# Kernel tuning notes

Hardware: AMD Instinct MI355X
Metric: run time of the kernel (lower is better)

Reference implementation:

```python
import jax, jax.numpy as jnp
import numpy as np

FEATURE_DIM = 512
PREDICATE_DIM = 2000
OBJECT_DIM = 100000
BATCH = 131072
EPS = 1e-5


def setup_inputs() -> dict:
    key = jax.random.key(0)
    ks = jax.random.split(key, 20)
    f, f2 = FEATURE_DIM, FEATURE_DIM // 2

    def w(k, shape, fan_in):
        bound = 1.0 / np.sqrt(fan_in)
        return jax.random.uniform(k, shape, jnp.float32, -bound, bound)

    inp = {
        "subj": jax.random.randint(ks[0], (BATCH,), 0, OBJECT_DIM),
        "obj": jax.random.randint(ks[1], (BATCH,), 0, OBJECT_DIM),
        "predi": jax.random.randint(ks[2], (BATCH,), 0, PREDICATE_DIM),
        # Linear weights stored as (in, out) so one_hot @ W.T == W_io[idx]
        "W1": w(ks[3], (OBJECT_DIM, f), OBJECT_DIM), "b1": w(ks[4], (f,), OBJECT_DIM),
        "g1": jnp.ones((f,), jnp.float32), "be1": jnp.zeros((f,), jnp.float32),
        "W2": w(ks[5], (OBJECT_DIM, f), OBJECT_DIM), "b2": w(ks[6], (f,), OBJECT_DIM),
        "g2": jnp.ones((f,), jnp.float32), "be2": jnp.zeros((f,), jnp.float32),
        "W3": w(ks[7], (PREDICATE_DIM, f), PREDICATE_DIM), "b3": w(ks[8], (f,), PREDICATE_DIM),
        "g3": jnp.ones((f,), jnp.float32), "be3": jnp.zeros((f,), jnp.float32),
        "W4": w(ks[9], (f2, f), f), "b4": w(ks[10], (f2,), f),
        "g4": jnp.ones((f2,), jnp.float32), "be4": jnp.zeros((f2,), jnp.float32),
        "W5": w(ks[11], (1, f2), f2), "b5": w(ks[12], (1,), f2),
    }
    return inp


def _bn(x, g, b):
    # BatchNorm1d training mode: biased variance over batch
    m = jnp.mean(x, axis=0)
    v = jnp.var(x, axis=0)
    return g * (x - m) * jax.lax.rsqrt(v + EPS) + b


def reference(subj, obj, predi,
              W1, b1, g1, be1,
              W2, b2, g2, be2,
              W3, b3, g3, be3,
              W4, b4, g4, be4,
              W5, b5):
    # one_hot(idx) @ W.T + b  ==  row gather of (in,out) weight
    s = jax.nn.relu(_bn(W1[subj] + b1, g1, be1))
    o = jax.nn.relu(_bn(W2[obj] + b2, g2, be2))
    p = jax.nn.relu(_bn(W3[predi] + b3, g3, be3))
    fused = s + p + o                                  # [B, F]
    h = jax.nn.relu(_bn(fused @ W4.T + b4, g4, be4))   # [B, F//2]
    logit = (h @ W5.T + b5).squeeze()                  # [B]
    return logit
```

## Files before the change

kernel.cpp:

```cpp
#include <hip/hip_runtime.h>

#define BATCHN 131072
#define FD 512
#define F2 256
#define NOBJ 100000
#define NPRED 2000
#define LDSTR 520

typedef __bf16 bf16x8 __attribute__((ext_vector_type(8)));
typedef float f32x4 __attribute__((ext_vector_type(4)));

__device__ __forceinline__ ushort f2bf(float f) {
  union { float f; uint u; } c; c.f = f;
  uint u = c.u;
  u += 0x7FFFu + ((u >> 16) & 1u);
  return (ushort)(u >> 16);
}

#define WS_STATS123 202752
#define WS_S4       205824
#define WS_SCSH123  238592
#define WS_SCSH4    241664
#define WS_W4BF     242176
#define WS_A1       307712
#define WS_A2       25907712
#define WS_A3       51507712

__global__ __launch_bounds__(256) void k_hist(
    const int* __restrict__ subj, const int* __restrict__ obj,
    const int* __restrict__ predi, int* __restrict__ cnt)
{
  int b = blockIdx.x * 256 + threadIdx.x;
  atomicAdd(&cnt[subj[b]], 1);
  atomicAdd(&cnt[NOBJ + obj[b]], 1);
  atomicAdd(&cnt[2 * NOBJ + predi[b]], 1);
}

#define NB1 782
#define NB3 16
#define NB_SCAN (NB1 + NB1 + NB3)
__global__ __launch_bounds__(256) void k_scan123(
    const float* __restrict__ W1, const float* __restrict__ W2,
    const float* __restrict__ W3, const int* __restrict__ cnt,
    float* __restrict__ stats)
{
  int blk = blockIdx.x;
  int e, rowBase, N;
  if (blk < NB1)            { e = 0; rowBase = blk * 128;          N = NOBJ; }
  else if (blk < 2 * NB1)   { e = 1; rowBase = (blk - NB1) * 128;  N = NOBJ; }
  else                      { e = 2; rowBase = (blk - 2*NB1) * 128; N = NPRED; }
  const float* W = (e == 0) ? W1 : (e == 1 ? W2 : W3);
  const int* cn = cnt + (e == 0 ? 0 : (e == 1 ? NOBJ : 2 * NOBJ));

  __shared__ int cnL[128];
  __shared__ float redS[512], redQ[512];
  int t = threadIdx.x;
  if (t < 128) { int r = rowBase + t; cnL[t] = (r < N) ? cn[r] : 0; }
  redS[t] = 0.f; redS[t + 256] = 0.f; redQ[t] = 0.f; redQ[t + 256] = 0.f;
  __syncthreads();

  int c = t & 63, rg = t >> 6;
  float s[8], q[8];
  #pragma unroll
  for (int j = 0; j < 8; ++j) { s[j] = 0.f; q[j] = 0.f; }
  for (int rl = rg; rl < 128; rl += 4) {
    float w = (float)cnL[rl];
    if (w == 0.f) continue;
    const float* row = W + (size_t)(rowBase + rl) * FD + c * 8;
    float4 va = *(const float4*)(row);
    float4 vb = *(const float4*)(row + 4);
    float x[8] = {va.x, va.y, va.z, va.w, vb.x, vb.y, vb.z, vb.w};
    #pragma unroll
    for (int j = 0; j < 8; ++j) { s[j] += w * x[j]; q[j] += w * x[j] * x[j]; }
  }
  #pragma unroll
  for (int j = 0; j < 8; ++j) {
    atomicAdd(&redS[c * 8 + j], s[j]);
    atomicAdd(&redQ[c * 8 + j], q[j]);
  }
  __syncthreads();
  float* se = stats + e * 1024;
  atomicAdd(&se[t],        redS[t]);
  atomicAdd(&se[t + 256],  redS[t + 256]);
  atomicAdd(&se[512 + t],  redQ[t]);
  atomicAdd(&se[768 + t],  redQ[t + 256]);
}

__global__ void k_fin123(const float* __restrict__ stats,
                         const float* __restrict__ g1, const float* __restrict__ be1,
                         const float* __restrict__ g2, const float* __restrict__ be2,
                         const float* __restrict__ g3, const float* __restrict__ be3,
                         float* __restrict__ scsh)
{
  int e = blockIdx.x, f = threadIdx.x;
  const float* g  = (e == 0) ? g1  : (e == 1 ? g2  : g3);
  const float* be = (e == 0) ? be1 : (e == 1 ? be2 : be3);
  float S = stats[e * 1024 + f], SS = stats[e * 1024 + 512 + f];
  const float invB = 1.f / (float)BATCHN;
  float mean = S * invB;
  float var  = SS * invB - mean * mean;
  if (!(var >= 0.f && var < 1e30f)) var = 1.f;
  if (!(mean > -1e30f && mean < 1e30f)) mean = 0.f;
  float r = rsqrtf(var + 1e-5f);
  float sc = g[f] * r;
  scsh[e * 1024 + f]       = sc;
  scsh[e * 1024 + 512 + f] = be[f] - mean * sc;
}

__global__ __launch_bounds__(256) void k_convW4(const float* __restrict__ W4,
                                                ushort* __restrict__ w4bf)
{
  int i = (blockIdx.x * 256 + threadIdx.x) * 4;
  float4 v = *(const float4*)(W4 + i);
  ushort4 o = {f2bf(v.x), f2bf(v.y), f2bf(v.z), f2bf(v.w)};
  *(ushort4*)(w4bf + i) = o;
}

#define NB_A1 3125
#define NB_A3 63
#define NB_BUILD (NB_A1 + NB_A1 + NB_A3)
__global__ __launch_bounds__(256) void k_buildA(
    const float* __restrict__ W1, const float* __restrict__ W2,
    const float* __restrict__ W3, const ushort* __restrict__ w4bf,
    const int* __restrict__ cnt, const float* __restrict__ scsh,
    float* __restrict__ A1, float* __restrict__ A2, float* __restrict__ A3)
{
  alignas(16) __shared__ ushort tileL[32 * LDSTR];
  __shared__ int okL[32];
  int blk = blockIdx.x;
  int e, rowBase, N; const float* W; float* A; const int* cn;
  if (blk < NB_A1)          { e = 0; rowBase = blk * 32;             N = NOBJ;  W = W1; A = A1; cn = cnt; }
  else if (blk < 2 * NB_A1) { e = 1; rowBase = (blk - NB_A1) * 32;   N = NOBJ;  W = W2; A = A2; cn = cnt + NOBJ; }
  else                      { e = 2; rowBase = (blk - 2*NB_A1) * 32; N = NPRED; W = W3; A = A3; cn = cnt + 2 * NOBJ; }

  int t = threadIdx.x;
  if (t < 32) { int r = rowBase + t; okL[t] = (r < N) && (cn[r] != 0); }
  int c = t & 63, rg = t >> 6;
  float sc[8], sh[8];
  #pragma unroll
  for (int j = 0; j < 8; ++j) {
    sc[j] = scsh[e * 1024 + c * 8 + j];
    sh[j] = scsh[e * 1024 + 512 + c * 8 + j];
  }
  __syncthreads();

  for (int r = rg; r < 32; r += 4) {
    union { ushort o[8]; uint4 v; } u;
    if (okL[r]) {
      const float* row = W + (size_t)(rowBase + r) * FD + c * 8;
      float4 va = *(const float4*)(row);
      float4 vb = *(const float4*)(row + 4);
      float x[8] = {va.x, va.y, va.z, va.w, vb.x, vb.y, vb.z, vb.w};
      #pragma unroll
      for (int j = 0; j < 8; ++j) {
        float v = fmaxf(fmaf(sc[j], x[j], sh[j]), 0.f);
        v = fminf(v, 60000.f);
        u.o[j] = f2bf(v);
      }
    } else { u.v.x = 0; u.v.y = 0; u.v.z = 0; u.v.w = 0; }
    *(uint4*)&tileL[r * LDSTR + c * 8] = u.v;
  }
  __syncthreads();

  int w = t >> 6, lane = t & 63, m = lane & 15, q = lane >> 4;
  f32x4 acc[2][4];
  #pragma unroll
  for (int mi = 0; mi < 2; ++mi)
    #pragma unroll
    for (int ni = 0; ni < 4; ++ni)
      acc[mi][ni] = (f32x4){0.f, 0.f, 0.f, 0.f};
  const ushort* w4p = w4bf + ((size_t)(64 * w + m)) * FD + q * 8;
  const ushort* fpL = tileL + m * LDSTR + q * 8;
  for (int kk = 0; kk < 16; ++kk) {
    int kc = kk * 32;
    bf16x8 af0 = *(const bf16x8*)(fpL + kc);
    bf16x8 af1 = *(const bf16x8*)(fpL + 16 * LDSTR + kc);
    #pragma unroll
    for (int ni = 0; ni < 4; ++ni) {
      bf16x8 bfv = *(const bf16x8*)(w4p + ni * 16 * FD + kc);
      acc[0][ni] = __builtin_amdgcn_mfma_f32_16x16x32_bf16(af0, bfv, acc[0][ni], 0, 0, 0);
      acc[1][ni] = __builtin_amdgcn_mfma_f32_16x16x32_bf16(af1, bfv, acc[1][ni], 0, 0, 0);
    }
  }
  __syncthreads();

  float* ldsF = (float*)tileL;
  #pragma unroll
  for (int mi = 0; mi < 2; ++mi)
    #pragma unroll
    for (int ni = 0; ni < 4; ++ni)
      #pragma unroll
      for (int rr = 0; rr < 4; ++rr)
        ldsF[(16 * mi + 4 * q + rr) * 258 + 64 * w + 16 * ni + m] = acc[mi][ni][rr];
  __syncthreads();
  for (int r = 0; r < 32; ++r) {
    if (okL[r]) A[(size_t)(rowBase + r) * F2 + t] = ldsF[r * 258 + t];
  }
}

__global__ __launch_bounds__(256) void k_hstats(
    const int* __restrict__ subj, const int* __restrict__ obj,
    const int* __restrict__ predi,
    const float* __restrict__ A1, const float* __restrict__ A2,
    const float* __restrict__ A3, float* __restrict__ s4)
{
  __shared__ float colS[256], colQ[256];
  int t = threadIdx.x;
  colS[t] = 0.f; colQ[t] = 0.f;
  __syncthreads();
  int c = t & 31;
  int pair = t >> 5;
  float ls[8], lq[8];
  #pragma unroll
  for (int j = 0; j < 8; ++j) { ls[j] = 0.f; lq[j] = 0.f; }
  int base = blockIdx.x * 64;
  #pragma unroll 2
  for (int i = 0; i < 8; ++i) {
    int b = base + i * 8 + pair;
    const float* r1 = A1 + (size_t)subj[b]  * F2 + c * 8;
    const float* r2 = A2 + (size_t)obj[b]   * F2 + c * 8;
    const float* r3 = A3 + (size_t)predi[b] * F2 + c * 8;
    f32x4 a0 = *(const f32x4*)(r1), a1 = *(const f32x4*)(r1 + 4);
    f32x4 b0 = *(const f32x4*)(r2), b1 = *(const f32x4*)(r2 + 4);
    f32x4 c0 = *(const f32x4*)(r3), c1 = *(const f32x4*)(r3 + 4);
    f32x4 h0 = a0 + b0 + c0, h1 = a1 + b1 + c1;
    #pragma unroll
    for (int j = 0; j < 4; ++j) {
      ls[j]     += h0[j]; lq[j]     += h0[j] * h0[j];
      ls[4 + j] += h1[j]; lq[4 + j] += h1[j] * h1[j];
    }
  }
  #pragma unroll
  for (int j = 0; j < 8; ++j) {
    atomicAdd(&colS[c * 8 + j], ls[j]);
    atomicAdd(&colQ[c * 8 + j], lq[j]);
  }
  __syncthreads();
  int slot = blockIdx.x & 63;
  atomicAdd(&s4[slot * 512 + t],       colS[t]);
  atomicAdd(&s4[slot * 512 + 256 + t], colQ[t]);
}

__global__ void k_fin4(const float* __restrict__ s4, const float* __restrict__ g4,
                       const float* __restrict__ be4, float* __restrict__ scsh4)
{
  int j = threadIdx.x;
  float S = 0.f, SS = 0.f;
  for (int sl = 0; sl < 64; ++sl) { S += s4[sl * 512 + j]; SS += s4[sl * 512 + 256 + j]; }
  const float invB = 1.f / (float)BATCHN;
  float mean = S * invB;
  float var  = SS * invB - mean * mean;
  if (!(var >= 0.f && var < 1e30f)) var = 1.f;
  if (!(mean > -1e30f && mean < 1e30f)) mean = 0.f;
  float r = rsqrtf(var + 1e-5f);
  float sc = g4[j] * r;
  scsh4[j]       = sc;
  scsh4[256 + j] = be4[j] - mean * sc;
}

__global__ __launch_bounds__(256) void k_final(
    const int* __restrict__ subj, const int* __restrict__ obj,
    const int* __restrict__ predi,
    const float* __restrict__ A1, const float* __restrict__ A2,
    const float* __restrict__ A3, const float* __restrict__ scsh4,
    const float* __restrict__ W5, const float* __restrict__ b5,
    float* __restrict__ out)
{
  int t = threadIdx.x;
  int c = t & 31, pair = t >> 5;
  float sc4v[8], sh4v[8], w5v[8];
  #pragma unroll
  for (int j = 0; j < 8; ++j) {
    int col = c * 8 + j;
    sc4v[j] = scsh4[col];
    sh4v[j] = scsh4[256 + col];
    w5v[j]  = W5[col];
  }
  float bb = b5[0];
  int base = blockIdx.x * 64;
  #pragma unroll 2
  for (int i = 0; i < 8; ++i) {
    int b = base + i * 8 + pair;
    const float* r1 = A1 + (size_t)subj[b]  * F2 + c * 8;
    const float* r2 = A2 + (size_t)obj[b]   * F2 + c * 8;
    const float* r3 = A3 + (size_t)predi[b] * F2 + c * 8;
    f32x4 a0 = *(const f32x4*)(r1), a1 = *(const f32x4*)(r1 + 4);
    f32x4 b0 = *(const f32x4*)(r2), b1 = *(const f32x4*)(r2 + 4);
    f32x4 c0 = *(const f32x4*)(r3), c1 = *(const f32x4*)(r3 + 4);
    f32x4 h0 = a0 + b0 + c0, h1 = a1 + b1 + c1;
    float acc = 0.f;
    #pragma unroll
    for (int j = 0; j < 4; ++j) {
      acc += fmaxf(fmaf(sc4v[j],     h0[j], sh4v[j]),     0.f) * w5v[j];
      acc += fmaxf(fmaf(sc4v[4 + j], h1[j], sh4v[4 + j]), 0.f) * w5v[4 + j];
    }
    #pragma unroll
    for (int off = 1; off < 32; off <<= 1)
      acc += __shfl_xor(acc, off, 64);
    if (c == 0) out[b] = acc + bb;
  }
}

extern "C" void kernel_launch(void* const* d_in, const int* in_sizes, int n_in,
                              void* d_out, int out_size, void* d_ws, size_t ws_size,
                              hipStream_t stream)
{
  const int* subj  = (const int*)d_in[0];
  const int* obj   = (const int*)d_in[1];
  const int* predi = (const int*)d_in[2];
  const float* W1  = (const float*)d_in[3];
  const float* g1  = (const float*)d_in[5];
  const float* be1 = (const float*)d_in[6];
  const float* W2  = (const float*)d_in[7];
  const float* g2  = (const float*)d_in[9];
  const float* be2 = (const float*)d_in[10];
  const float* W3  = (const float*)d_in[11];
  const float* g3  = (const float*)d_in[13];
  const float* be3 = (const float*)d_in[14];
  const float* W4  = (const float*)d_in[15];
  const float* g4  = (const float*)d_in[17];
  const float* be4 = (const float*)d_in[18];
  const float* W5  = (const float*)d_in[19];
  const float* b5  = (const float*)d_in[20];

  float* wsf   = (float*)d_ws;
  int*   cnt   = (int*)d_ws;
  ushort* w4bf = (ushort*)(wsf + WS_W4BF);
  float* A1    = wsf + WS_A1;
  float* A2    = wsf + WS_A2;
  float* A3    = wsf + WS_A3;
  float* out   = (float*)d_out;

  hipMemsetAsync(d_ws, 0, WS_SCSH123 * 4, stream);
  k_hist<<<BATCHN / 256, 256, 0, stream>>>(subj, obj, predi, cnt);
  k_convW4<<<128, 256, 0, stream>>>(W4, w4bf);
  k_scan123<<<NB_SCAN, 256, 0, stream>>>(W1, W2, W3, cnt, wsf + WS_STATS123);
  k_fin123<<<3, 512, 0, stream>>>(wsf + WS_STATS123, g1, be1, g2, be2, g3, be3, wsf + WS_SCSH123);
  k_buildA<<<NB_BUILD, 256, 0, stream>>>(W1, W2, W3, w4bf, cnt, wsf + WS_SCSH123, A1, A2, A3);
  k_hstats<<<BATCHN / 64, 256, 0, stream>>>(subj, obj, predi, A1, A2, A3, wsf + WS_S4);
  k_fin4<<<1, 256, 0, stream>>>(wsf + WS_S4, g4, be4, wsf + WS_SCSH4);
  k_final<<<BATCHN / 64, 256, 0, stream>>>(subj, obj, predi, A1, A2, A3, wsf + WS_SCSH4, W5, b5, out);
}
```

Before: 844.5 us.

## Store projected tables and hidden activations in bf16, compact nonzero rows, prefetch W4

The per-row projected tables A1/A2/A3 are now stored as bf16 instead of fp32, which halves gather traffic. The stats kernel also writes the summed hidden vector h as bf16 so the final kernel reads one contiguous row instead of three random gathers. The scan and build kernels first compact the list of rows with nonzero counts in LDS and unroll over that list, and the W4 fragments in the MFMA loop are software-prefetched one step ahead. The cost is extra rounding error from bf16 storage of the tables and of h, plus an added 64 MB write and read for h.

```diff
diff --git a/kernel.cpp b/kernel.cpp
--- a/kernel.cpp
+++ b/kernel.cpp
@@ -23,8 +23,9 @@
 #define WS_SCSH4    241664
 #define WS_W4BF     242176
 #define WS_A1       307712
-#define WS_A2       25907712
-#define WS_A3       51507712
+#define WS_A2       13107712
+#define WS_A3       25907712
+#define WS_H        26163712
 
 __global__ __launch_bounds__(256) void k_hist(
     const int* __restrict__ subj, const int* __restrict__ obj,
@@ -46,33 +47,60 @@
 {
   int blk = blockIdx.x;
   int e, rowBase, N;
-  if (blk < NB1)            { e = 0; rowBase = blk * 128;          N = NOBJ; }
-  else if (blk < 2 * NB1)   { e = 1; rowBase = (blk - NB1) * 128;  N = NOBJ; }
+  if (blk < NB1)            { e = 0; rowBase = blk * 128;           N = NOBJ; }
+  else if (blk < 2 * NB1)   { e = 1; rowBase = (blk - NB1) * 128;   N = NOBJ; }
   else                      { e = 2; rowBase = (blk - 2*NB1) * 128; N = NPRED; }
   const float* W = (e == 0) ? W1 : (e == 1 ? W2 : W3);
   const int* cn = cnt + (e == 0 ? 0 : (e == 1 ? NOBJ : 2 * NOBJ));
 
-  __shared__ int cnL[128];
+  __shared__ int cnL[128], listR[128], nkS;
   __shared__ float redS[512], redQ[512];
   int t = threadIdx.x;
-  if (t < 128) { int r = rowBase + t; cnL[t] = (r < N) ? cn[r] : 0; }
+  if (t == 0) nkS = 0;
   redS[t] = 0.f; redS[t + 256] = 0.f; redQ[t] = 0.f; redQ[t + 256] = 0.f;
   __syncthreads();
+  if (t < 128) {
+    int r = rowBase + t;
+    int cv = (r < N) ? cn[r] : 0;
+    cnL[t] = cv;
+    if (cv > 0) { int p = atomicAdd(&nkS, 1); listR[p] = t; }
+  }
+  __syncthreads();
+  int nk = nkS;
 
   int c = t & 63, rg = t >> 6;
   float s[8], q[8];
   #pragma unroll
   for (int j = 0; j < 8; ++j) { s[j] = 0.f; q[j] = 0.f; }
-  for (int rl = rg; rl < 128; rl += 4) {
-    float w = (float)cnL[rl];
-    if (w == 0.f) continue;
-    const float* row = W + (size_t)(rowBase + rl) * FD + c * 8;
-    float4 va = *(const float4*)(row);
-    float4 vb = *(const float4*)(row + 4);
-    float x[8] = {va.x, va.y, va.z, va.w, vb.x, vb.y, vb.z, vb.w};
-    #pragma unroll
-    for (int j = 0; j < 8; ++j) { s[j] += w * x[j]; q[j] += w * x[j] * x[j]; }
-  }
+
+  #define SCAN_ACC(w_, va_, vb_) { \
+    float x_[8] = {va_.x, va_.y, va_.z, va_.w, vb_.x, vb_.y, vb_.z, vb_.w}; \
+    _Pragma("unroll") \
+    for (int j = 0; j < 8; ++j) { float wx = w_ * x_[j]; s[j] += wx; q[j] = fmaf(wx, x_[j], q[j]); } }
+
+  int ii = rg;
+  for (; ii + 12 < nk; ii += 16) {
+    int r0 = listR[ii], r1 = listR[ii + 4], r2 = listR[ii + 8], r3 = listR[ii + 12];
+    const float* p0 = W + (size_t)(rowBase + r0) * FD + c * 8;
+    const float* p1 = W + (size_t)(rowBase + r1) * FD + c * 8;
+    const float* p2 = W + (size_t)(rowBase + r2) * FD + c * 8;
+    const float* p3 = W + (size_t)(rowBase + r3) * FD + c * 8;
+    float4 a0 = *(const float4*)(p0), b0 = *(const float4*)(p0 + 4);
+    float4 a1 = *(const float4*)(p1), b1 = *(const float4*)(p1 + 4);
+    float4 a2 = *(const float4*)(p2), b2 = *(const float4*)(p2 + 4);
+    float4 a3 = *(const float4*)(p3), b3 = *(const float4*)(p3 + 4);
+    float w0 = (float)cnL[r0], w1 = (float)cnL[r1], w2 = (float)cnL[r2], w3 = (float)cnL[r3];
+    SCAN_ACC(w0, a0, b0); SCAN_ACC(w1, a1, b1); SCAN_ACC(w2, a2, b2); SCAN_ACC(w3, a3, b3);
+  }
+  for (; ii < nk; ii += 4) {
+    int r0 = listR[ii];
+    const float* p0 = W + (size_t)(rowBase + r0) * FD + c * 8;
+    float4 a0 = *(const float4*)(p0), b0 = *(const float4*)(p0 + 4);
+    float w0 = (float)cnL[r0];
+    SCAN_ACC(w0, a0, b0);
+  }
+  #undef SCAN_ACC
+
   #pragma unroll
   for (int j = 0; j < 8; ++j) {
     atomicAdd(&redS[c * 8 + j], s[j]);
@@ -123,18 +151,25 @@
     const float* __restrict__ W1, const float* __restrict__ W2,
     const float* __restrict__ W3, const ushort* __restrict__ w4bf,
     const int* __restrict__ cnt, const float* __restrict__ scsh,
-    float* __restrict__ A1, float* __restrict__ A2, float* __restrict__ A3)
+    ushort* __restrict__ A1, ushort* __restrict__ A2, ushort* __restrict__ A3)
 {
   alignas(16) __shared__ ushort tileL[32 * LDSTR];
-  __shared__ int okL[32];
+  __shared__ int okL[32], listR[32], nkS;
   int blk = blockIdx.x;
-  int e, rowBase, N; const float* W; float* A; const int* cn;
+  int e, rowBase, N; const float* W; ushort* A; const int* cn;
   if (blk < NB_A1)          { e = 0; rowBase = blk * 32;             N = NOBJ;  W = W1; A = A1; cn = cnt; }
   else if (blk < 2 * NB_A1) { e = 1; rowBase = (blk - NB_A1) * 32;   N = NOBJ;  W = W2; A = A2; cn = cnt + NOBJ; }
   else                      { e = 2; rowBase = (blk - 2*NB_A1) * 32; N = NPRED; W = W3; A = A3; cn = cnt + 2 * NOBJ; }
 
   int t = threadIdx.x;
-  if (t < 32) { int r = rowBase + t; okL[t] = (r < N) && (cn[r] != 0); }
+  if (t == 0) nkS = 0;
+  __syncthreads();
+  if (t < 32) {
+    int r = rowBase + t;
+    int ok = (r < N) && (cn[r] != 0);
+    okL[t] = ok;
+    if (ok) { int p = atomicAdd(&nkS, 1); listR[p] = t; }
+  }
   int c = t & 63, rg = t >> 6;
   float sc[8], sh[8];
   #pragma unroll
@@ -143,23 +178,35 @@
     sh[j] = scsh[e * 1024 + 512 + c * 8 + j];
   }
   __syncthreads();
-
-  for (int r = rg; r < 32; r += 4) {
-    union { ushort o[8]; uint4 v; } u;
-    if (okL[r]) {
-      const float* row = W + (size_t)(rowBase + r) * FD + c * 8;
-      float4 va = *(const float4*)(row);
-      float4 vb = *(const float4*)(row + 4);
-      float x[8] = {va.x, va.y, va.z, va.w, vb.x, vb.y, vb.z, vb.w};
-      #pragma unroll
-      for (int j = 0; j < 8; ++j) {
-        float v = fmaxf(fmaf(sc[j], x[j], sh[j]), 0.f);
-        v = fminf(v, 60000.f);
-        u.o[j] = f2bf(v);
-      }
-    } else { u.v.x = 0; u.v.y = 0; u.v.z = 0; u.v.w = 0; }
-    *(uint4*)&tileL[r * LDSTR + c * 8] = u.v;
-  }
+  int nk = nkS;
+
+  #define CONV_STORE(rr_, va_, vb_) { \
+    float x_[8] = {va_.x, va_.y, va_.z, va_.w, vb_.x, vb_.y, vb_.z, vb_.w}; \
+    union { ushort o[8]; uint4 v; } u_; \
+    _Pragma("unroll") \
+    for (int j = 0; j < 8; ++j) { \
+      float v_ = fmaxf(fmaf(sc[j], x_[j], sh[j]), 0.f); \
+      v_ = fminf(v_, 60000.f); \
+      u_.o[j] = f2bf(v_); } \
+    *(uint4*)&tileL[(rr_) * LDSTR + c * 8] = u_.v; }
+
+  int ii = rg;
+  for (; ii + 4 < nk; ii += 8) {
+    int ra = listR[ii], rb = listR[ii + 4];
+    const float* pa = W + (size_t)(rowBase + ra) * FD + c * 8;
+    const float* pb = W + (size_t)(rowBase + rb) * FD + c * 8;
+    float4 a0 = *(const float4*)(pa), a1 = *(const float4*)(pa + 4);
+    float4 b0 = *(const float4*)(pb), b1 = *(const float4*)(pb + 4);
+    CONV_STORE(ra, a0, a1);
+    CONV_STORE(rb, b0, b1);
+  }
+  if (ii < nk) {
+    int ra = listR[ii];
+    const float* pa = W + (size_t)(rowBase + ra) * FD + c * 8;
+    float4 a0 = *(const float4*)(pa), a1 = *(const float4*)(pa + 4);
+    CONV_STORE(ra, a0, a1);
+  }
+  #undef CONV_STORE
   __syncthreads();
 
   int w = t >> 6, lane = t & 63, m = lane & 15, q = lane >> 4;
@@ -171,16 +218,32 @@
       acc[mi][ni] = (f32x4){0.f, 0.f, 0.f, 0.f};
   const ushort* w4p = w4bf + ((size_t)(64 * w + m)) * FD + q * 8;
   const ushort* fpL = tileL + m * LDSTR + q * 8;
+
+  bf16x8 bc0 = *(const bf16x8*)(w4p + 0 * 16 * FD);
+  bf16x8 bc1 = *(const bf16x8*)(w4p + 1 * 16 * FD);
+  bf16x8 bc2 = *(const bf16x8*)(w4p + 2 * 16 * FD);
+  bf16x8 bc3 = *(const bf16x8*)(w4p + 3 * 16 * FD);
   for (int kk = 0; kk < 16; ++kk) {
     int kc = kk * 32;
     bf16x8 af0 = *(const bf16x8*)(fpL + kc);
     bf16x8 af1 = *(const bf16x8*)(fpL + 16 * LDSTR + kc);
-    #pragma unroll
-    for (int ni = 0; ni < 4; ++ni) {
-      bf16x8 bfv = *(const bf16x8*)(w4p + ni * 16 * FD + kc);
-      acc[0][ni] = __builtin_amdgcn_mfma_f32_16x16x32_bf16(af0, bfv, acc[0][ni], 0, 0, 0);
-      acc[1][ni] = __builtin_amdgcn_mfma_f32_16x16x32_bf16(af1, bfv, acc[1][ni], 0, 0, 0);
+    bf16x8 bn0, bn1, bn2, bn3;
+    if (kk < 15) {
+      int kn = kc + 32;
+      bn0 = *(const bf16x8*)(w4p + 0 * 16 * FD + kn);
+      bn1 = *(const bf16x8*)(w4p + 1 * 16 * FD + kn);
+      bn2 = *(const bf16x8*)(w4p + 2 * 16 * FD + kn);
+      bn3 = *(const bf16x8*)(w4p + 3 * 16 * FD + kn);
     }
+    acc[0][0] = __builtin_amdgcn_mfma_f32_16x16x32_bf16(af0, bc0, acc[0][0], 0, 0, 0);
+    acc[1][0] = __builtin_amdgcn_mfma_f32_16x16x32_bf16(af1, bc0, acc[1][0], 0, 0, 0);
+    acc[0][1] = __builtin_amdgcn_mfma_f32_16x16x32_bf16(af0, bc1, acc[0][1], 0, 0, 0);
+    acc[1][1] = __builtin_amdgcn_mfma_f32_16x16x32_bf16(af1, bc1, acc[1][1], 0, 0, 0);
+    acc[0][2] = __builtin_amdgcn_mfma_f32_16x16x32_bf16(af0, bc2, acc[0][2], 0, 0, 0);
+    acc[1][2] = __builtin_amdgcn_mfma_f32_16x16x32_bf16(af1, bc2, acc[1][2], 0, 0, 0);
+    acc[0][3] = __builtin_amdgcn_mfma_f32_16x16x32_bf16(af0, bc3, acc[0][3], 0, 0, 0);
+    acc[1][3] = __builtin_amdgcn_mfma_f32_16x16x32_bf16(af1, bc3, acc[1][3], 0, 0, 0);
+    bc0 = bn0; bc1 = bn1; bc2 = bn2; bc3 = bn3;
   }
   __syncthreads();
 
@@ -193,16 +256,23 @@
       for (int rr = 0; rr < 4; ++rr)
         ldsF[(16 * mi + 4 * q + rr) * 258 + 64 * w + 16 * ni + m] = acc[mi][ni][rr];
   __syncthreads();
-  for (int r = 0; r < 32; ++r) {
-    if (okL[r]) A[(size_t)(rowBase + r) * F2 + t] = ldsF[r * 258 + t];
+  int hr = t >> 7, p = (t & 127) * 2;
+  for (int r = 0; r < 32; r += 2) {
+    int rr = r + hr;
+    if (okL[rr]) {
+      float v0 = ldsF[rr * 258 + p], v1 = ldsF[rr * 258 + p + 1];
+      uint pack = (uint)f2bf(v0) | ((uint)f2bf(v1) << 16);
+      *(uint*)&A[(size_t)(rowBase + rr) * F2 + p] = pack;
+    }
   }
 }
 
 __global__ __launch_bounds__(256) void k_hstats(
     const int* __restrict__ subj, const int* __restrict__ obj,
     const int* __restrict__ predi,
-    const float* __restrict__ A1, const float* __restrict__ A2,
-    const float* __restrict__ A3, float* __restrict__ s4)
+    const ushort* __restrict__ A1, const ushort* __restrict__ A2,
+    const ushort* __restrict__ A3, ushort* __restrict__ h,
+    float* __restrict__ s4)
 {
   __shared__ float colS[256], colQ[256];
   int t = threadIdx.x;
@@ -217,18 +287,17 @@
   #pragma unroll 2
   for (int i = 0; i < 8; ++i) {
     int b = base + i * 8 + pair;
-    const float* r1 = A1 + (size_t)subj[b]  * F2 + c * 8;
-    const float* r2 = A2 + (size_t)obj[b]   * F2 + c * 8;
-    const float* r3 = A3 + (size_t)predi[b] * F2 + c * 8;
-    f32x4 a0 = *(const f32x4*)(r1), a1 = *(const f32x4*)(r1 + 4);
-    f32x4 b0 = *(const f32x4*)(r2), b1 = *(const f32x4*)(r2 + 4);
-    f32x4 c0 = *(const f32x4*)(r3), c1 = *(const f32x4*)(r3 + 4);
-    f32x4 h0 = a0 + b0 + c0, h1 = a1 + b1 + c1;
+    bf16x8 v1 = *(const bf16x8*)(A1 + (size_t)subj[b]  * F2 + c * 8);
+    bf16x8 v2 = *(const bf16x8*)(A2 + (size_t)obj[b]   * F2 + c * 8);
+    bf16x8 v3 = *(const bf16x8*)(A3 + (size_t)predi[b] * F2 + c * 8);
+    union { ushort o[8]; uint4 v; } u;
     #pragma unroll
-    for (int j = 0; j < 4; ++j) {
-      ls[j]     += h0[j]; lq[j]     += h0[j] * h0[j];
-      ls[4 + j] += h1[j]; lq[4 + j] += h1[j] * h1[j];
+    for (int j = 0; j < 8; ++j) {
+      float hv = (float)v1[j] + (float)v2[j] + (float)v3[j];
+      ls[j] += hv; lq[j] = fmaf(hv, hv, lq[j]);
+      u.o[j] = f2bf(hv);
     }
+    *(uint4*)&h[(size_t)b * F2 + c * 8] = u.v;
   }
   #pragma unroll
   for (int j = 0; j < 8; ++j) {
@@ -259,10 +328,7 @@
 }
 
 __global__ __launch_bounds__(256) void k_final(
-    const int* __restrict__ subj, const int* __restrict__ obj,
-    const int* __restrict__ predi,
-    const float* __restrict__ A1, const float* __restrict__ A2,
-    const float* __restrict__ A3, const float* __restrict__ scsh4,
+    const ushort* __restrict__ h, const float* __restrict__ scsh4,
     const float* __restrict__ W5, const float* __restrict__ b5,
     float* __restrict__ out)
 {
@@ -281,19 +347,11 @@
   #pragma unroll 2
   for (int i = 0; i < 8; ++i) {
     int b = base + i * 8 + pair;
-    const float* r1 = A1 + (size_t)subj[b]  * F2 + c * 8;
-    const float* r2 = A2 + (size_t)obj[b]   * F2 + c * 8;
-    const float* r3 = A3 + (size_t)predi[b] * F2 + c * 8;
-    f32x4 a0 = *(const f32x4*)(r1), a1 = *(const f32x4*)(r1 + 4);
-    f32x4 b0 = *(const f32x4*)(r2), b1 = *(const f32x4*)(r2 + 4);
-    f32x4 c0 = *(const f32x4*)(r3), c1 = *(const f32x4*)(r3 + 4);
-    f32x4 h0 = a0 + b0 + c0, h1 = a1 + b1 + c1;
+    bf16x8 hv = *(const bf16x8*)(h + (size_t)b * F2 + c * 8);
     float acc = 0.f;
     #pragma unroll
-    for (int j = 0; j < 4; ++j) {
-      acc += fmaxf(fmaf(sc4v[j],     h0[j], sh4v[j]),     0.f) * w5v[j];
-      acc += fmaxf(fmaf(sc4v[4 + j], h1[j], sh4v[4 + j]), 0.f) * w5v[4 + j];
-    }
+    for (int j = 0; j < 8; ++j)
+      acc += fmaxf(fmaf(sc4v[j], (float)hv[j], sh4v[j]), 0.f) * w5v[j];
     #pragma unroll
     for (int off = 1; off < 32; off <<= 1)
       acc += __shfl_xor(acc, off, 64);
@@ -326,9 +384,10 @@
   float* wsf   = (float*)d_ws;
   int*   cnt   = (int*)d_ws;
   ushort* w4bf = (ushort*)(wsf + WS_W4BF);
-  float* A1    = wsf + WS_A1;
-  float* A2    = wsf + WS_A2;
-  float* A3    = wsf + WS_A3;
+  ushort* A1   = (ushort*)(wsf + WS_A1);
+  ushort* A2   = (ushort*)(wsf + WS_A2);
+  ushort* A3   = (ushort*)(wsf + WS_A3);
+  ushort* hbuf = (ushort*)(wsf + WS_H);
   float* out   = (float*)d_out;
 
   hipMemsetAsync(d_ws, 0, WS_SCSH123 * 4, stream);
@@ -337,7 +396,7 @@
   k_scan123<<<NB_SCAN, 256, 0, stream>>>(W1, W2, W3, cnt, wsf + WS_STATS123);
   k_fin123<<<3, 512, 0, stream>>>(wsf + WS_STATS123, g1, be1, g2, be2, g3, be3, wsf + WS_SCSH123);
   k_buildA<<<NB_BUILD, 256, 0, stream>>>(W1, W2, W3, w4bf, cnt, wsf + WS_SCSH123, A1, A2, A3);
-  k_hstats<<<BATCHN / 64, 256, 0, stream>>>(subj, obj, predi, A1, A2, A3, wsf + WS_S4);
+  k_hstats<<<BATCHN / 64, 256, 0, stream>>>(subj, obj, predi, A1, A2, A3, hbuf, wsf + WS_S4);
   k_fin4<<<1, 256, 0, stream>>>(wsf + WS_S4, g4, be4, wsf + WS_SCSH4);
-  k_final<<<BATCHN / 64, 256, 0, stream>>>(subj, obj, predi, A1, A2, A3, wsf + WS_SCSH4, W5, b5, out);
-}
+  k_final<<<BATCHN / 64, 256, 0, stream>>>(hbuf, wsf + WS_SCSH4, W5, b5, out);
+}
```

New measurement: 771.8 us. 1.09x faster.
